# Kernel tuning notes

Measured on AMD Instinct MI355X. Metric: run time of the kernel, lower is better.

The kernel has to match this reference:

```python
import jax, jax.numpy as jnp
import numpy as np

NB, NC, IN, HID, OUT, ENG = 8, 16384, 64, 128, 64, 128
SYNC, DEBATE = 0.15, 0.15


def setup_inputs() -> dict:
    key = jax.random.key(0)
    ks = jax.random.split(key, 24)
    rn = lambda k, s, sc=0.05: jax.random.normal(k, s, jnp.float32) * sc
    return {
        "x": jax.random.normal(ks[0], (1, IN), jnp.float32),
        "noise": jax.random.normal(ks[1], (NB, 1, IN), jnp.float32),
        "amps": jax.random.uniform(ks[2], (NB,), jnp.float32, 0.5, 1.5),
        "hiddens": jax.random.normal(ks[3], (NB, NC, HID), jnp.float32) * 0.1,
        "eaW1": rn(ks[4], (ENG, IN + HID)), "eaB1": rn(ks[5], (ENG,)),
        "eaW2": rn(ks[6], (OUT, ENG)), "eaB2": rn(ks[7], (OUT,)),
        "egW1": rn(ks[8], (ENG, IN + HID)), "egB1": rn(ks[9], (ENG,)),
        "egW2": rn(ks[10], (OUT, ENG)), "egB2": rn(ks[11], (OUT,)),
        "gru_Wih": rn(ks[12], (3 * HID, OUT + 1)), "gru_Whh": rn(ks[13], (3 * HID, HID)),
        "gru_bih": rn(ks[14], (3 * HID,)), "gru_bhh": rn(ks[15], (3 * HID,)),
        "headW": rn(ks[16], (IN, OUT)), "headb": rn(ks[17], (IN,)),
        "mixW": rn(ks[18], (HID, HID * NB)), "mixb": rn(ks[19], (HID,)),
        "step": 10,
    }


def reference(x, noise, amps, hiddens, eaW1, eaB1, eaW2, eaB2,
              egW1, egB1, egW2, egB2, gru_Wih, gru_Whh, gru_bih, gru_bhh,
              headW, headb, mixW, mixb, step):
    sg = jax.lax.stop_gradient
    # per-branch perturbed input, broadcast over cells
    scale = 0.05 * jnp.arange(1, NB + 1, dtype=x.dtype)[:, None, None]
    xb = jnp.broadcast_to(x[None] + noise * scale, (NB, NC, IN))
    comb = jnp.concatenate([xb, hiddens], axis=-1)          # (NB,NC,IN+HID)
    a = jax.nn.relu(comb @ eaW1.T + eaB1) @ eaW2.T + eaB2
    g = jax.nn.relu(comb @ egW1.T + egB1) @ egW2.T + egB2
    out = a - g                                             # (NB,NC,OUT)
    tension = jnp.mean(out ** 2, axis=-1)                   # (NB,NC)

    # GRUCell update (mem input is detached in the original)
    mem_in = sg(jnp.concatenate([out, tension[..., None]], axis=-1))
    gi = mem_in @ gru_Wih.T + gru_bih                       # (NB,NC,3H)
    gh = hiddens @ gru_Whh.T + gru_bhh
    ir, iz, inn = jnp.split(gi, 3, axis=-1)
    hr, hz, hn = jnp.split(gh, 3, axis=-1)
    r = jax.nn.sigmoid(ir + hr)
    z = jax.nn.sigmoid(iz + hz)
    n = jnp.tanh(inn + r * hn)
    newh = sg((1.0 - z) * n + z * hiddens)                  # stored detached

    # faction sync + debate (state only)
    nf = min(8, NC // 2)
    fs = NC // nf
    core = newh[:, :nf * fs].reshape(NB, nf, fs, HID)
    core = (1.0 - SYNC) * core + SYNC * core.mean(axis=2, keepdims=True)
    if step > 5:
        glob = core.mean(axis=2).mean(axis=1)               # (NB,HID)
        dc = max(1, fs // 4)
        core = core.at[:, :, :dc].set(
            (1.0 - DEBATE) * core[:, :, :dc] + DEBATE * glob[:, None, None, :])
    newh = jnp.concatenate([core.reshape(NB, nf * fs, HID), newh[:, nf * fs:]], axis=1)

    # amplitude-weighted branch combine (amps used via .item() -> constants)
    aabs = jnp.abs(amps)
    aabs = aabs / (aabs.sum() + 1e-8)
    cell_out = jnp.einsum('b,bnd->nd', sg(aabs), out)       # (NC,OUT)
    avg_t = tension.mean(axis=0)                            # (NC,)
    w = jax.nn.softmax(sg(avg_t))                           # weights from .item()'d tensions
    combined = (w[:, None] * cell_out).sum(axis=0, keepdims=True)  # (1,OUT)
    pred = combined @ headW.T + headb                       # (1,IN)

    # interference mixer state update on branch 0
    interf = newh.mean(axis=1).reshape(1, -1) @ mixW.T + mixb       # (1,HID)
    newh = newh.at[0].add(sg(interf) * 0.05)

    return pred, avg_t.mean(), newh
```

## Files before the change

kernel.cpp:

```cpp
#include <hip/hip_runtime.h>
#include <math.h>

#define NB   8
#define NCC  16384
#define HID  128

typedef __attribute__((ext_vector_type(8))) short short8;
typedef __attribute__((ext_vector_type(4))) float f32x4;

#define MFMA(a,b,c) __builtin_amdgcn_mfma_f32_16x16x32_bf16(a,b,c,0,0,0)

#define WS_AABS   0
#define WS_BASE1  8
#define WS_BOUT   2056
#define WS_BSUMR  2120
#define WS_BSUMZ  2248
#define WS_BIHN   2376
#define WS_BHHN   2504
#define WS_W64    2632
#define WS_INTERF 3024
#define WS_FRAG   3152
#define WS_SD     64592
#define WS_AVGT   73808
#define WS_TS     90192
#define WS_FMEAN  221264
#define WS_PART2  230480
#define WS_FPART  246864
#define WS_CO     771152
#define WS_PARTE  1819728
#define WS_PARTA  1819984

__device__ __forceinline__ unsigned short f2b(float f) {
    unsigned int u = __float_as_uint(f);
    unsigned int r = (u + 0x7fffu + ((u >> 16) & 1u)) >> 16;
    return (unsigned short)r;
}
__device__ __forceinline__ float b2f(unsigned short us) {
    return __uint_as_float(((unsigned int)us) << 16);
}
__device__ __forceinline__ float sigm(float x) {
    return __builtin_amdgcn_rcpf(1.f + __expf(-x));
}
__device__ __forceinline__ float tanh_fast(float x) {
    return 1.f - 2.f * __builtin_amdgcn_rcpf(__expf(2.f * x) + 1.f);
}
__device__ __forceinline__ unsigned int cvtpk(float lo, float hi) {
    unsigned int r;
    asm volatile("v_cvt_pk_bf16_f32 %0, %1, %2" : "=v"(r) : "v"(lo), "v"(hi));
    return r;
}
__device__ __forceinline__ void stg(char* dst, int row, int cb, float4 u, float4 v) {
    uint4 pk = make_uint4(cvtpk(u.x, u.y), cvtpk(u.z, u.w),
                          cvtpk(v.x, v.y), cvtpk(v.z, v.w));
    *(uint4*)(dst + row * 256 + (cb ^ ((row & 7) << 4))) = pk;
}

__global__ __launch_bounds__(1024) void kprep(
    const float* __restrict__ x, const float* __restrict__ noise,
    const float* __restrict__ amps,
    const float* __restrict__ eaW1, const float* __restrict__ eaB1,
    const float* __restrict__ egW1, const float* __restrict__ egB1,
    const float* __restrict__ eaW2, const float* __restrict__ eaB2,
    const float* __restrict__ egW2, const float* __restrict__ egB2,
    const float* __restrict__ gWih, const float* __restrict__ gWhh,
    const float* __restrict__ gbih, const float* __restrict__ gbhh,
    float* __restrict__ ws)
{
    int i = blockIdx.x * 1024 + threadIdx.x;
    if (i < 122880) {
        short* wsh = (short*)(ws + WS_FRAG);
        float v;
        if (i < 32768) {
            int rel = i;
            int j = rel & 7, l = (rel >> 3) & 63, tk = rel >> 9;
            int kt = tk & 3, nt = tk >> 2;
            int n = nt * 16 + (l & 15), k = kt * 32 + ((l >> 4) << 3) + j;
            v = (n < 128) ? eaW1[n * 192 + 64 + k] : egW1[(n - 128) * 192 + 64 + k];
        } else if (i < 49152) {
            int rel = i - 32768;
            int j = rel & 7, l = (rel >> 3) & 63, tk = rel >> 9;
            int kt = tk & 7, nt = tk >> 3;
            int d = nt * 16 + (l & 15), k = kt * 32 + ((l >> 4) << 3) + j;
            v = (k < 128) ? eaW2[d * 128 + k] : -egW2[d * 128 + (k - 128)];
        } else if (i < 73728) {
            int rel = i - 49152;
            int j = rel & 7, l = (rel >> 3) & 63, tk = rel >> 9;
            int kt = tk & 1, nt = tk >> 1;
            int r = nt * 16 + (l & 15), k = kt * 32 + ((l >> 4) << 3) + j;
            v = gWih[r * 65 + k];
        } else {
            int rel = i - 73728;
            int j = rel & 7, l = (rel >> 3) & 63, tk = rel >> 9;
            int kt = tk & 3, nt = tk >> 2;
            int r = nt * 16 + (l & 15), k = kt * 32 + ((l >> 4) << 3) + j;
            v = gWhh[r * 128 + k];
        }
        wsh[i] = (short)f2b(v);
    }
    if (blockIdx.x == 0) {
        __shared__ float xb[8][64];
        int t = threadIdx.x;
        if (t < 512) {
            int b = t >> 6, k = t & 63;
            xb[b][k] = x[k] + noise[b * 64 + k] * (0.05f * (float)(b + 1));
        }
        if (t == 0) {
            float s = 0.f;
            for (int b = 0; b < 8; b++) s += fabsf(amps[b]);
            s += 1e-8f;
            for (int b = 0; b < 8; b++) ws[WS_AABS + b] = fabsf(amps[b]) / s;
        }
        __syncthreads();
        for (int ii = t; ii < 2048; ii += 1024) {
            int b = ii >> 8, n = ii & 255;
            const float* Wp; float s;
            if (n < 128) { Wp = eaW1 + n * 192; s = eaB1[n]; }
            else         { Wp = egW1 + (n - 128) * 192; s = egB1[n - 128]; }
            for (int k = 0; k < 64; k++) s += xb[b & 7][k] * Wp[k];
            ws[WS_BASE1 + ii] = s;
        }
        if (t < 64) ws[WS_BOUT + t] = eaB2[t] - egB2[t];
        if (t < 128) {
            ws[WS_BSUMR + t] = gbih[t] + gbhh[t];
            ws[WS_BSUMZ + t] = gbih[128 + t] + gbhh[128 + t];
            ws[WS_BIHN + t]  = gbih[256 + t];
            ws[WS_BHHN + t]  = gbhh[256 + t];
        }
        if (t < 384) ws[WS_W64 + t] = gWih[t * 65 + 64];
    }
}

__global__ __launch_bounds__(1024) void kA(
    const float* __restrict__ hiddens, float* __restrict__ newh,
    float* __restrict__ ws)
{
    __shared__ char  wlds[98304];
    __shared__ char  hsb[64 * 256];
    __shared__ char  agb[64 * 512];
    __shared__ float ts_s[64];
    __shared__ float tsum_s[64];

    const int t    = threadIdx.x;
    const int lane = t & 63;
    const int w    = t >> 6;
    const int rg   = w >> 2;
    const int nq   = w & 3;
    const int col  = lane & 15;
    const int kq   = lane >> 4;
    const int r0   = rg * 16;
    const int n0   = blockIdx.x * 64;

    {
        const float4* src = (const float4*)(ws + WS_FRAG);
        float4* dst = (float4*)wlds;
#pragma unroll
        for (int p = 0; p < 6; p++) dst[p * 1024 + t] = src[p * 1024 + t];
    }
    const short8* W1F = (const short8*)wlds;
    const short8* W2F = (const short8*)(wlds + 65536);

    const float bo = ws[WS_BOUT + nq * 16 + col];
    float co_reg[4];
#pragma unroll
    for (int i = 0; i < 4; i++) co_reg[i] = 0.f;
    if (t < 64) tsum_s[t] = 0.f;

    const int flat = t * 8;
    const int srow = flat >> 7;
    const int scb  = (flat & 127) * 2;

    {
        const float* hs = hiddens + (size_t)n0 * HID;
        float4 a0 = *(const float4*)(hs + flat);
        float4 a1 = *(const float4*)(hs + flat + 4);
        stg(hsb, srow, scb, a0, a1);
    }
    float4 pfa0, pfa1;
    unsigned short* outu = (unsigned short*)newh;

    for (int b = 0; b < NB; ++b) {
        __syncthreads();
        if (t < 64) {
            if (b > 0) {
                ws[WS_TS + (size_t)(b - 1) * NCC + n0 + t] = ts_s[t];
                tsum_s[t] += ts_s[t];
            }
            ts_s[t] = 0.f;
        }
        if (b < 7) {
            const float* hsn = hiddens + ((size_t)((b + 1) * NCC + n0)) * HID;
            pfa0 = *(const float4*)(hsn + flat);
            pfa1 = *(const float4*)(hsn + flat + 4);
        }

        {
            short8 aH[4];
#pragma unroll
            for (int ks = 0; ks < 4; ks++) {
                int row = r0 + col;
                aH[ks] = *(const short8*)(hsb + row * 256 +
                           ((ks * 64 + (kq << 4)) ^ ((row & 7) << 4)));
            }
#pragma unroll
            for (int nti = 0; nti < 4; nti++) {
                int nt = nq * 4 + nti;
                f32x4 ac = {0.f, 0.f, 0.f, 0.f};
#pragma unroll
                for (int kt = 0; kt < 4; kt++)
                    ac = MFMA(aH[kt], W1F[(nt * 4 + kt) * 64 + lane], ac);
                int n = nt * 16 + col;
                float bs = ws[WS_BASE1 + b * 256 + n];
#pragma unroll
                for (int j = 0; j < 4; j++) {
                    int row = r0 + (kq << 2) + j;
                    float v = fmaxf(ac[j] + bs, 0.f);
                    *(unsigned short*)(agb + row * 512 +
                        ((n * 2) ^ ((row & 7) << 4))) = f2b(v);
                }
            }
        }
        __syncthreads();

        if (b < 7) stg(hsb, srow, scb, pfa0, pfa1);

        {
            f32x4 ov = {0.f, 0.f, 0.f, 0.f};
#pragma unroll
            for (int kt = 0; kt < 8; kt++) {
                int kb = kt * 64 + (kq << 4);
                int ra = r0 + col;
                short8 a0 = *(const short8*)(agb + ra * 512 + (kb ^ ((ra & 7) << 4)));
                ov = MFMA(a0, W2F[(nq * 8 + kt) * 64 + lane], ov);
            }
            int d = nq * 16 + col;
            float aab = ws[WS_AABS + b];
#pragma unroll
            for (int j = 0; j < 4; j++) {
                int row = r0 + (kq << 2) + j;
                float v = ov[j] + bo;
                co_reg[j] += aab * v;
                outu[(size_t)(b * NCC + n0 + row) * 256 + 192 + d] = f2b(v);
                float sq = v * v;
                sq += __shfl_xor(sq, 1);
                sq += __shfl_xor(sq, 2);
                sq += __shfl_xor(sq, 4);
                sq += __shfl_xor(sq, 8);
                if (col == 0) atomicAdd(&ts_s[row], sq);
            }
        }
    }
    __syncthreads();
    if (t < 64) {
        ws[WS_TS + (size_t)7 * NCC + n0 + t] = ts_s[t];
        tsum_s[t] += ts_s[t];
        ws[WS_AVGT + n0 + t] = tsum_s[t] * (1.f / 512.f);
    }
    {
        int d = nq * 16 + col;
#pragma unroll
        for (int j = 0; j < 4; j++) {
            int row = r0 + (kq << 2) + j;
            ws[WS_CO + (size_t)(n0 + row) * 64 + d] = co_reg[j];
        }
    }
}

__global__ __launch_bounds__(1024) void kB(
    const float* __restrict__ hiddens, float* __restrict__ newh,
    float* __restrict__ ws)
{
    __shared__ char  wl[147456];
    __shared__ char  hsb[32 * 256];
    __shared__ char  otb[32 * 128];
    __shared__ float ts_s[32];
    __shared__ float fp2[2][128];

    const int t    = threadIdx.x;
    const int lane = t & 63;
    const int w    = t >> 6;
    const int rh   = w >> 3;
    const int hg   = w & 7;
    const int col  = lane & 15;
    const int kq   = lane >> 4;
    const int chunk = blockIdx.x;
    const int n0   = chunk * 32;

    {
        const float4* src = (const float4*)(ws + WS_FRAG) + 6144;
        float4* dst = (float4*)wl;
#pragma unroll
        for (int p = 0; p < 9; p++) dst[p * 1024 + t] = src[p * 1024 + t];
    }
    const short8* WIHF = (const short8*)wl;
    const short8* WHHF = (const short8*)(wl + 49152);
    const unsigned short* outu = (const unsigned short*)newh;

    const int h = hg * 16 + col;
    const float bsr = ws[WS_BSUMR + h];
    const float bsz = ws[WS_BSUMZ + h];
    const float bin = ws[WS_BIHN + h];
    const float bhn = ws[WS_BHHN + h];
    const float wr  = ws[WS_W64 + h];
    const float wz  = ws[WS_W64 + 128 + h];
    const float wn  = ws[WS_W64 + 256 + h];

    const int flat = t * 8;
    const int srow = flat >> 7;
    const int scb  = (flat & 127) * 2;
    const int ocell = t >> 4;
    const int ooff  = (t & 15) * 4;

    float4 rh0 = {0,0,0,0}, rh1 = {0,0,0,0};
    uint2  ro = make_uint2(0, 0);
    float  rts = 0.f;
    if (t < 512) {
        const float* hs = hiddens + (size_t)n0 * HID;
        rh0 = *(const float4*)(hs + flat);
        rh1 = *(const float4*)(hs + flat + 4);
        ro  = *(const uint2*)(outu + (size_t)(n0 + ocell) * 256 + 192 + ooff);
    }
    if (t < 32) rts = ws[WS_TS + n0 + t];

    for (int b = 0; b < NB; ++b) {
        if (t < 512) {
            stg(hsb, srow, scb, rh0, rh1);
            *(uint2*)(otb + ocell * 128 + ((ooff * 2) ^ ((ocell & 7) << 4))) = ro;
        }
        if (t < 32) ts_s[t] = rts;
        __syncthreads();

        if (b < 7) {
            if (t < 512) {
                const float* hsn = hiddens + ((size_t)((b + 1) * NCC + n0)) * HID;
                rh0 = *(const float4*)(hsn + flat);
                rh1 = *(const float4*)(hsn + flat + 4);
                ro  = *(const uint2*)(outu + (size_t)((b + 1) * NCC + n0 + ocell) * 256 + 192 + ooff);
            }
            if (t < 32) rts = ws[WS_TS + (size_t)(b + 1) * NCC + n0 + t];
        }

        {
            float* nbase = newh + ((size_t)(b * NCC + n0)) * HID;
            const int ra = rh * 16 + col;
            f32x4 R = {0.f,0.f,0.f,0.f};
            f32x4 Z = {0.f,0.f,0.f,0.f};
            f32x4 I = {0.f,0.f,0.f,0.f};
            f32x4 N = {0.f,0.f,0.f,0.f};
#pragma unroll
            for (int ks = 0; ks < 2; ks++) {
                short8 a0 = *(const short8*)(otb + ra * 128 +
                             ((ks * 64 + (kq << 4)) ^ ((ra & 7) << 4)));
                R = MFMA(a0, WIHF[(hg * 2 + ks) * 64 + lane], R);
                Z = MFMA(a0, WIHF[((hg + 8) * 2 + ks) * 64 + lane], Z);
                I = MFMA(a0, WIHF[((hg + 16) * 2 + ks) * 64 + lane], I);
            }
#pragma unroll
            for (int ks = 0; ks < 4; ks++) {
                short8 a0 = *(const short8*)(hsb + ra * 256 +
                             ((ks * 64 + (kq << 4)) ^ ((ra & 7) << 4)));
                R = MFMA(a0, WHHF[(hg * 4 + ks) * 64 + lane], R);
                Z = MFMA(a0, WHHF[((hg + 8) * 4 + ks) * 64 + lane], Z);
                N = MFMA(a0, WHHF[((hg + 16) * 4 + ks) * 64 + lane], N);
            }
            float flsum = 0.f;
#pragma unroll
            for (int j = 0; j < 4; j++) {
                int row = rh * 16 + (kq << 2) + j;
                float tv = ts_s[row] * (1.f / 64.f);
                float r  = sigm(R[j] + bsr + tv * wr);
                float z  = sigm(Z[j] + bsz + tv * wz);
                float hn = N[j] + bhn;
                float nn = tanh_fast(I[j] + bin + tv * wn + r * hn);
                float hold = b2f(*(const unsigned short*)(hsb + row * 256 +
                                 ((h * 2) ^ ((row & 7) << 4))));
                float nh = (1.f - z) * nn + z * hold;
                nbase[(size_t)row * HID + h] = nh;
                flsum += nh;
            }
            flsum += __shfl_xor(flsum, 16);
            flsum += __shfl_xor(flsum, 32);
            if (kq == 0) fp2[rh][h] = flsum;
        }
        __syncthreads();

        if (t < 128)
            ws[WS_FPART + ((size_t)(b * 512 + chunk)) * 128 + t] = fp2[0][t] + fp2[1][t];
    }
}

__global__ __launch_bounds__(128) void k2_fmean(float* __restrict__ ws)
{
    int bf = blockIdx.x;
    int b = bf >> 3, f = bf & 7;
    int h = threadIdx.x;
    float s = 0.f, s8 = 0.f;
    for (int j = 0; j < 64; j++) {
        float v = ws[WS_FPART + ((size_t)(b * 512 + f * 64 + j)) * 128 + h];
        s += v;
        if (j < 16) s8 += v;
    }
    ws[WS_FMEAN + (b * 8 + f) * 128 + h] = s * (1.f / 2048.f);
    ws[WS_SD + (b * 8 + f) * 128 + h] = s8;
}

__global__ __launch_bounds__(256) void k4mv(
    const float* __restrict__ mixW, const float* __restrict__ mixb,
    const int* __restrict__ step, float* __restrict__ ws)
{
    __shared__ float hm[1024];
    __shared__ float red[256];
    int h0 = blockIdx.x, t = threadIdx.x;
    bool deb = (step[0] > 5);
    for (int j = t; j < 1024; j += 256) {
        int b = j >> 7, hh = j & 127;
        float s = 0.f, sd = 0.f;
        for (int f = 0; f < 8; f++) {
            s  += ws[WS_FMEAN + (b * 8 + f) * 128 + hh];
            sd += ws[WS_SD + (b * 8 + f) * 128 + hh];
        }
        float gl = s * 0.125f;
        float tot = 16384.f * gl;
        if (deb) tot += 0.15f * (3481.6f * gl - 0.85f * sd);
        hm[j] = tot * (1.f / 16384.f);
    }
    __syncthreads();
    float4 wv = *(const float4*)(mixW + (size_t)h0 * 1024 + t * 4);
    float4 hv = *(const float4*)(&hm[t * 4]);
    float s = wv.x * hv.x + wv.y * hv.y + wv.z * hv.z + wv.w * hv.w;
    red[t] = s; __syncthreads();
    for (int st = 128; st > 0; st >>= 1) { if (t < st) red[t] += red[t + st]; __syncthreads(); }
    if (t == 0) ws[WS_INTERF + h0] = mixb[h0] + red[0];
}

__global__ __launch_bounds__(256) void k35_blend(
    float* __restrict__ newh, const float* __restrict__ ws,
    const int* __restrict__ step)
{
    int blk = blockIdx.x;
    int b = blk >> 8, ck = blk & 255;
    int t = threadIdx.x;
    int h4 = t & 31;
    int cg = t >> 5;
    int base = ck * 64;
    int f = base >> 11;
    bool deb = (step[0] > 5) && ((base & 2047) < 512);
    float4 fm = *(const float4*)(ws + WS_FMEAN + (size_t)(b * 8 + f) * 128 + h4 * 4);
    float glx = 0.f, gly = 0.f, glz = 0.f, glw = 0.f;
    for (int ff = 0; ff < 8; ff++) {
        float4 v = *(const float4*)(ws + WS_FMEAN + (size_t)(b * 8 + ff) * 128 + h4 * 4);
        glx += v.x; gly += v.y; glz += v.z; glw += v.w;
    }
    glx *= 0.125f; gly *= 0.125f; glz *= 0.125f; glw *= 0.125f;
    float4 itf = {0.f, 0.f, 0.f, 0.f};
    if (b == 0) {
        float4 iv = *(const float4*)(ws + WS_INTERF + h4 * 4);
        itf.x = 0.05f * iv.x; itf.y = 0.05f * iv.y;
        itf.z = 0.05f * iv.z; itf.w = 0.05f * iv.w;
    }
    for (int i = 0; i < 8; i++) {
        int cell = base + i * 8 + cg;
        size_t idx = ((size_t)b * NCC + cell) * 128 + h4 * 4;
        float4 v = *(float4*)(newh + idx);
        v.x = 0.85f * v.x + 0.15f * fm.x;
        v.y = 0.85f * v.y + 0.15f * fm.y;
        v.z = 0.85f * v.z + 0.15f * fm.z;
        v.w = 0.85f * v.w + 0.15f * fm.w;
        if (deb) {
            v.x = 0.85f * v.x + 0.15f * glx;
            v.y = 0.85f * v.y + 0.15f * gly;
            v.z = 0.85f * v.z + 0.15f * glz;
            v.w = 0.85f * v.w + 0.15f * glw;
        }
        v.x += itf.x; v.y += itf.y; v.z += itf.z; v.w += itf.w;
        *(float4*)(newh + idx) = v;
    }
}

__global__ __launch_bounds__(256) void kred(float* __restrict__ ws)
{
    __shared__ float wexp[64];
    __shared__ float red[256];
    int blk = blockIdx.x, t = threadIdx.x;
    int n0 = blk * 64;
    float av = 0.f;
    if (t < 64) {
        av = ws[WS_AVGT + n0 + t];
        wexp[t] = __expf(av);
    }
    __syncthreads();
    int d = t & 63, q = t >> 6;
    float s = 0.f;
    for (int i = 0; i < 16; i++) {
        int c = q * 16 + i;
        s += wexp[c] * ws[WS_CO + (size_t)(n0 + c) * 64 + d];
    }
    red[t] = s; __syncthreads();
    if (t < 64)
        ws[WS_PART2 + blk * 64 + t] = red[t] + red[64 + t] + red[128 + t] + red[192 + t];
    if (t < 64) {
        float e = wexp[t], a2 = av;
        e  += __shfl_xor(e, 1);  a2 += __shfl_xor(a2, 1);
        e  += __shfl_xor(e, 2);  a2 += __shfl_xor(a2, 2);
        e  += __shfl_xor(e, 4);  a2 += __shfl_xor(a2, 4);
        e  += __shfl_xor(e, 8);  a2 += __shfl_xor(a2, 8);
        e  += __shfl_xor(e, 16); a2 += __shfl_xor(a2, 16);
        e  += __shfl_xor(e, 32); a2 += __shfl_xor(a2, 32);
        if (t == 0) { ws[WS_PARTE + blk] = e; ws[WS_PARTA + blk] = a2; }
    }
}

__global__ __launch_bounds__(256) void kpred(
    const float* __restrict__ headW, const float* __restrict__ headb,
    float* __restrict__ ws, float* __restrict__ d_out)
{
    __shared__ float red[256];
    __shared__ float num[64];
    __shared__ float den_s;
    int t = threadIdx.x;
    int d = t & 63, q = t >> 6;
    float s = 0.f;
    for (int i = 0; i < 64; i++) s += ws[WS_PART2 + (q * 64 + i) * 64 + d];
    red[t] = s; __syncthreads();
    if (t < 64) num[t] = red[t] + red[64 + t] + red[128 + t] + red[192 + t];
    __syncthreads();
    red[t] = ws[WS_PARTE + t]; __syncthreads();
    for (int st = 128; st > 0; st >>= 1) { if (t < st) red[t] += red[t + st]; __syncthreads(); }
    if (t == 0) den_s = red[0];
    __syncthreads();
    red[t] = ws[WS_PARTA + t]; __syncthreads();
    for (int st = 128; st > 0; st >>= 1) { if (t < st) red[t] += red[t + st]; __syncthreads(); }
    if (t == 0) d_out[64] = red[0] * (1.f / (float)NCC);
    __syncthreads();
    if (t < 64) {
        float inv_den = 1.f / den_s;
        float p = headb[t];
        for (int d2 = 0; d2 < 64; d2++) p += (num[d2] * inv_den) * headW[t * 64 + d2];
        d_out[t] = p;
    }
}

extern "C" void kernel_launch(void* const* d_in, const int* in_sizes, int n_in,
                              void* d_out, int out_size, void* d_ws, size_t ws_size,
                              hipStream_t stream)
{
    const float* x       = (const float*)d_in[0];
    const float* noise   = (const float*)d_in[1];
    const float* amps    = (const float*)d_in[2];
    const float* hiddens = (const float*)d_in[3];
    const float* eaW1    = (const float*)d_in[4];
    const float* eaB1    = (const float*)d_in[5];
    const float* eaW2    = (const float*)d_in[6];
    const float* eaB2    = (const float*)d_in[7];
    const float* egW1    = (const float*)d_in[8];
    const float* egB1    = (const float*)d_in[9];
    const float* egW2    = (const float*)d_in[10];
    const float* egB2    = (const float*)d_in[11];
    const float* gWih    = (const float*)d_in[12];
    const float* gWhh    = (const float*)d_in[13];
    const float* gbih    = (const float*)d_in[14];
    const float* gbhh    = (const float*)d_in[15];
    const float* headW   = (const float*)d_in[16];
    const float* headb   = (const float*)d_in[17];
    const float* mixW    = (const float*)d_in[18];
    const float* mixb    = (const float*)d_in[19];
    const int*   step    = (const int*)d_in[20];

    float* out  = (float*)d_out;
    float* newh = out + 65;
    float* ws   = (float*)d_ws;

    kprep<<<120, 1024, 0, stream>>>(x, noise, amps, eaW1, eaB1, egW1, egB1,
                                    eaW2, eaB2, egW2, egB2, gWih, gWhh,
                                    gbih, gbhh, ws);
    kA<<<256, 1024, 0, stream>>>(hiddens, newh, ws);
    kB<<<512, 1024, 0, stream>>>(hiddens, newh, ws);
    k2_fmean<<<64, 128, 0, stream>>>(ws);
    k4mv<<<128, 256, 0, stream>>>(mixW, mixb, step, ws);
    k35_blend<<<2048, 256, 0, stream>>>(newh, ws, step);
    kred<<<256, 256, 0, stream>>>(ws);
    kpred<<<1, 256, 0, stream>>>(headW, headb, ws, out);
}
```

Before: 131.2 us.

## Double GRU tile to 64 cells per block, keep only Whh in LDS

kB now processes 64 cells per block instead of 32, and launches 256 blocks instead of 512. Each wave computes two hidden-column groups, and all 1024 threads take part in staging. Only the Whh fragments are copied into LDS; the Wih fragments are read straight from global memory (expected to hit in L2/cache). This halves the per-block weight-staging cost and the partial-sum traffic, with k2_fmean adjusted to match. The trade-offs are fewer blocks on the machine, more global loads inside the MFMA loop, and a longer serial section per wave.

```diff
diff --git a/kernel.cpp b/kernel.cpp
--- a/kernel.cpp
+++ b/kernel.cpp
@@ -269,40 +269,32 @@
     const float* __restrict__ hiddens, float* __restrict__ newh,
     float* __restrict__ ws)
 {
-    __shared__ char  wl[147456];
-    __shared__ char  hsb[32 * 256];
-    __shared__ char  otb[32 * 128];
-    __shared__ float ts_s[32];
-    __shared__ float fp2[2][128];
+    __shared__ char  wl[98304];
+    __shared__ char  hsb[64 * 256];
+    __shared__ char  otb[64 * 128];
+    __shared__ float ts_s[64];
+    __shared__ float fp4[4][128];
 
     const int t    = threadIdx.x;
     const int lane = t & 63;
     const int w    = t >> 6;
-    const int rh   = w >> 3;
-    const int hg   = w & 7;
+    const int rg   = w >> 2;
+    const int hq   = w & 3;
     const int col  = lane & 15;
     const int kq   = lane >> 4;
+    const int r0   = rg * 16;
     const int chunk = blockIdx.x;
-    const int n0   = chunk * 32;
+    const int n0   = chunk * 64;
 
     {
-        const float4* src = (const float4*)(ws + WS_FRAG) + 6144;
+        const float4* src = (const float4*)(ws + WS_FRAG) + 9216;
         float4* dst = (float4*)wl;
 #pragma unroll
-        for (int p = 0; p < 9; p++) dst[p * 1024 + t] = src[p * 1024 + t];
-    }
-    const short8* WIHF = (const short8*)wl;
-    const short8* WHHF = (const short8*)(wl + 49152);
+        for (int p = 0; p < 6; p++) dst[p * 1024 + t] = src[p * 1024 + t];
+    }
+    const short8* WHHF = (const short8*)wl;
+    const short8* WIHF = (const short8*)((const short*)(ws + WS_FRAG) + 49152);
     const unsigned short* outu = (const unsigned short*)newh;
-
-    const int h = hg * 16 + col;
-    const float bsr = ws[WS_BSUMR + h];
-    const float bsz = ws[WS_BSUMZ + h];
-    const float bin = ws[WS_BIHN + h];
-    const float bhn = ws[WS_BHHN + h];
-    const float wr  = ws[WS_W64 + h];
-    const float wz  = ws[WS_W64 + 128 + h];
-    const float wn  = ws[WS_W64 + 256 + h];
 
     const int flat = t * 8;
     const int srow = flat >> 7;
@@ -310,81 +302,90 @@
     const int ocell = t >> 4;
     const int ooff  = (t & 15) * 4;
 
-    float4 rh0 = {0,0,0,0}, rh1 = {0,0,0,0};
-    uint2  ro = make_uint2(0, 0);
+    float4 rh0, rh1;
+    uint2  ro;
     float  rts = 0.f;
-    if (t < 512) {
+    {
         const float* hs = hiddens + (size_t)n0 * HID;
         rh0 = *(const float4*)(hs + flat);
         rh1 = *(const float4*)(hs + flat + 4);
         ro  = *(const uint2*)(outu + (size_t)(n0 + ocell) * 256 + 192 + ooff);
     }
-    if (t < 32) rts = ws[WS_TS + n0 + t];
+    if (t < 64) rts = ws[WS_TS + n0 + t];
 
     for (int b = 0; b < NB; ++b) {
-        if (t < 512) {
-            stg(hsb, srow, scb, rh0, rh1);
-            *(uint2*)(otb + ocell * 128 + ((ooff * 2) ^ ((ocell & 7) << 4))) = ro;
-        }
-        if (t < 32) ts_s[t] = rts;
+        stg(hsb, srow, scb, rh0, rh1);
+        *(uint2*)(otb + ocell * 128 + ((ooff * 2) ^ ((ocell & 7) << 4))) = ro;
+        if (t < 64) ts_s[t] = rts;
         __syncthreads();
 
         if (b < 7) {
-            if (t < 512) {
-                const float* hsn = hiddens + ((size_t)((b + 1) * NCC + n0)) * HID;
-                rh0 = *(const float4*)(hsn + flat);
-                rh1 = *(const float4*)(hsn + flat + 4);
-                ro  = *(const uint2*)(outu + (size_t)((b + 1) * NCC + n0 + ocell) * 256 + 192 + ooff);
-            }
-            if (t < 32) rts = ws[WS_TS + (size_t)(b + 1) * NCC + n0 + t];
+            const float* hsn = hiddens + ((size_t)((b + 1) * NCC + n0)) * HID;
+            rh0 = *(const float4*)(hsn + flat);
+            rh1 = *(const float4*)(hsn + flat + 4);
+            ro  = *(const uint2*)(outu + (size_t)((b + 1) * NCC + n0 + ocell) * 256 + 192 + ooff);
+            if (t < 64) rts = ws[WS_TS + (size_t)(b + 1) * NCC + n0 + t];
         }
 
         {
             float* nbase = newh + ((size_t)(b * NCC + n0)) * HID;
-            const int ra = rh * 16 + col;
-            f32x4 R = {0.f,0.f,0.f,0.f};
-            f32x4 Z = {0.f,0.f,0.f,0.f};
-            f32x4 I = {0.f,0.f,0.f,0.f};
-            f32x4 N = {0.f,0.f,0.f,0.f};
-#pragma unroll
-            for (int ks = 0; ks < 2; ks++) {
-                short8 a0 = *(const short8*)(otb + ra * 128 +
-                             ((ks * 64 + (kq << 4)) ^ ((ra & 7) << 4)));
-                R = MFMA(a0, WIHF[(hg * 2 + ks) * 64 + lane], R);
-                Z = MFMA(a0, WIHF[((hg + 8) * 2 + ks) * 64 + lane], Z);
-                I = MFMA(a0, WIHF[((hg + 16) * 2 + ks) * 64 + lane], I);
+            const int ra = r0 + col;
+#pragma unroll
+            for (int hgi = 0; hgi < 2; hgi++) {
+                const int hg = hq * 2 + hgi;
+                const int h = hg * 16 + col;
+                f32x4 R = {0.f,0.f,0.f,0.f};
+                f32x4 Z = {0.f,0.f,0.f,0.f};
+                f32x4 I = {0.f,0.f,0.f,0.f};
+                f32x4 N = {0.f,0.f,0.f,0.f};
+#pragma unroll
+                for (int ks = 0; ks < 2; ks++) {
+                    short8 a0 = *(const short8*)(otb + ra * 128 +
+                                 ((ks * 64 + (kq << 4)) ^ ((ra & 7) << 4)));
+                    R = MFMA(a0, WIHF[(hg * 2 + ks) * 64 + lane], R);
+                    Z = MFMA(a0, WIHF[((hg + 8) * 2 + ks) * 64 + lane], Z);
+                    I = MFMA(a0, WIHF[((hg + 16) * 2 + ks) * 64 + lane], I);
+                }
+#pragma unroll
+                for (int ks = 0; ks < 4; ks++) {
+                    short8 a0 = *(const short8*)(hsb + ra * 256 +
+                                 ((ks * 64 + (kq << 4)) ^ ((ra & 7) << 4)));
+                    R = MFMA(a0, WHHF[(hg * 4 + ks) * 64 + lane], R);
+                    Z = MFMA(a0, WHHF[((hg + 8) * 4 + ks) * 64 + lane], Z);
+                    N = MFMA(a0, WHHF[((hg + 16) * 4 + ks) * 64 + lane], N);
+                }
+                const float bsr = ws[WS_BSUMR + h];
+                const float bsz = ws[WS_BSUMZ + h];
+                const float bin = ws[WS_BIHN + h];
+                const float bhn = ws[WS_BHHN + h];
+                const float wr  = ws[WS_W64 + h];
+                const float wz  = ws[WS_W64 + 128 + h];
+                const float wn  = ws[WS_W64 + 256 + h];
+                float flsum = 0.f;
+#pragma unroll
+                for (int j = 0; j < 4; j++) {
+                    int row = r0 + (kq << 2) + j;
+                    float tv = ts_s[row] * (1.f / 64.f);
+                    float r  = sigm(R[j] + bsr + tv * wr);
+                    float z  = sigm(Z[j] + bsz + tv * wz);
+                    float hn = N[j] + bhn;
+                    float nn = tanh_fast(I[j] + bin + tv * wn + r * hn);
+                    float hold = b2f(*(const unsigned short*)(hsb + row * 256 +
+                                     ((h * 2) ^ ((row & 7) << 4))));
+                    float nh = (1.f - z) * nn + z * hold;
+                    nbase[(size_t)row * HID + h] = nh;
+                    flsum += nh;
+                }
+                flsum += __shfl_xor(flsum, 16);
+                flsum += __shfl_xor(flsum, 32);
+                if (kq == 0) fp4[rg][h] = flsum;
             }
-#pragma unroll
-            for (int ks = 0; ks < 4; ks++) {
-                short8 a0 = *(const short8*)(hsb + ra * 256 +
-                             ((ks * 64 + (kq << 4)) ^ ((ra & 7) << 4)));
-                R = MFMA(a0, WHHF[(hg * 4 + ks) * 64 + lane], R);
-                Z = MFMA(a0, WHHF[((hg + 8) * 4 + ks) * 64 + lane], Z);
-                N = MFMA(a0, WHHF[((hg + 16) * 4 + ks) * 64 + lane], N);
-            }
-            float flsum = 0.f;
-#pragma unroll
-            for (int j = 0; j < 4; j++) {
-                int row = rh * 16 + (kq << 2) + j;
-                float tv = ts_s[row] * (1.f / 64.f);
-                float r  = sigm(R[j] + bsr + tv * wr);
-                float z  = sigm(Z[j] + bsz + tv * wz);
-                float hn = N[j] + bhn;
-                float nn = tanh_fast(I[j] + bin + tv * wn + r * hn);
-                float hold = b2f(*(const unsigned short*)(hsb + row * 256 +
-                                 ((h * 2) ^ ((row & 7) << 4))));
-                float nh = (1.f - z) * nn + z * hold;
-                nbase[(size_t)row * HID + h] = nh;
-                flsum += nh;
-            }
-            flsum += __shfl_xor(flsum, 16);
-            flsum += __shfl_xor(flsum, 32);
-            if (kq == 0) fp2[rh][h] = flsum;
         }
         __syncthreads();
 
         if (t < 128)
-            ws[WS_FPART + ((size_t)(b * 512 + chunk)) * 128 + t] = fp2[0][t] + fp2[1][t];
+            ws[WS_FPART + ((size_t)(b * 256 + chunk)) * 128 + t] =
+                fp4[0][t] + fp4[1][t] + fp4[2][t] + fp4[3][t];
     }
 }
 
@@ -394,10 +395,10 @@
     int b = bf >> 3, f = bf & 7;
     int h = threadIdx.x;
     float s = 0.f, s8 = 0.f;
-    for (int j = 0; j < 64; j++) {
-        float v = ws[WS_FPART + ((size_t)(b * 512 + f * 64 + j)) * 128 + h];
+    for (int j = 0; j < 32; j++) {
+        float v = ws[WS_FPART + ((size_t)(b * 256 + f * 32 + j)) * 128 + h];
         s += v;
-        if (j < 16) s8 += v;
+        if (j < 8) s8 += v;
     }
     ws[WS_FMEAN + (b * 8 + f) * 128 + h] = s * (1.f / 2048.f);
     ws[WS_SD + (b * 8 + f) * 128 + h] = s8;
@@ -573,7 +574,7 @@
                                     eaW2, eaB2, egW2, egB2, gWih, gWhh,
                                     gbih, gbhh, ws);
     kA<<<256, 1024, 0, stream>>>(hiddens, newh, ws);
-    kB<<<512, 1024, 0, stream>>>(hiddens, newh, ws);
+    kB<<<256, 1024, 0, stream>>>(hiddens, newh, ws);
     k2_fmean<<<64, 128, 0, stream>>>(ws);
     k4mv<<<128, 256, 0, stream>>>(mixW, mixb, step, ws);
     k35_blend<<<2048, 256, 0, stream>>>(newh, ws, step);
```

New measurement: 155.3 us. 1.18x slower.
